# Kernel optimization log

Measured on AMD Instinct MI355X. Metric: run time of the kernel, lower is better.

The kernel has to match this reference:

```python
import jax, jax.numpy as jnp
import numpy as np

N_NODES = 100000
N_EDGES = 1600000
D = 128
NEG_SLOPE = 0.2


def setup_inputs() -> dict:
    key = jax.random.key(0)
    k1, k2, k3, k4, k5, k6 = jax.random.split(key, 6)
    x = jax.random.normal(k1, (N_NODES, D), dtype=jnp.float32)
    src = jax.random.randint(k2, (N_EDGES,), 0, N_NODES)
    dst = jax.random.randint(k3, (N_EDGES,), 0, N_NODES)
    # torch.nn.Linear default init: U(-1/sqrt(fan_in), 1/sqrt(fan_in))
    W = jax.random.uniform(k4, (D, D), dtype=jnp.float32, minval=-1.0, maxval=1.0) / np.sqrt(D)
    a_left = jax.random.uniform(k5, (1, D), dtype=jnp.float32, minval=-1.0, maxval=1.0) / np.sqrt(D)
    a_right = jax.random.uniform(k6, (1, D), dtype=jnp.float32, minval=-1.0, maxval=1.0) / np.sqrt(D)
    return {"x": x, "src": src, "dst": dst, "W": W, "a_left": a_left, "a_right": a_right}


def reference(x, src, dst, W, a_left, a_right):
    n = x.shape[0]
    # node-wise projections
    h = x @ W.T                      # [N, D]
    e_l = h @ a_left.T               # [N, 1]
    e_r = h @ a_right.T              # [N, 1]
    # edge attention logits: u_add_v then leaky_relu
    e = e_l[src] + e_r[dst]          # [E, 1]
    e = jnp.where(e >= 0, e, NEG_SLOPE * e)
    # edge softmax over incoming edges of each destination node
    e = e[:, 0]
    m = jax.ops.segment_max(e, dst, num_segments=n)          # [N]
    m = jnp.where(jnp.isfinite(m), m, 0.0)                   # guard empty segments
    ex = jnp.exp(e - m[dst])                                 # [E]
    denom = jax.ops.segment_sum(ex, dst, num_segments=n)     # [N]
    alpha = ex / jnp.maximum(denom[dst], 1e-38)              # [E]
    # weighted aggregation: sum_e h[src] * alpha -> dst
    msg = h[src] * alpha[:, None]                            # [E, D]
    out = jax.ops.segment_sum(msg, dst, num_segments=n)      # [N, D]
    return out
```

## Files before the change

### kernel.cpp

```cpp
#include <hip/hip_runtime.h>
#include <math.h>

#define N_NODES 100000
#define N_EDGES 1600000
#define D 128
#define NEG_SLOPE_F 0.2f
#define BK 32
#define NB3 3125
#define ECAP 1024
#define BEPB 16384
#define NBINB 98

typedef short short8 __attribute__((ext_vector_type(8)));
typedef float f32x4 __attribute__((ext_vector_type(4)));

__device__ __forceinline__ unsigned short f2bf_rtn(float f) {
    unsigned int u = __float_as_uint(f);
    u += 0x7fffu + ((u >> 16) & 1u);
    return (unsigned short)(u >> 16);
}
__device__ __forceinline__ float bf2f(unsigned short h) {
    return __uint_as_float((unsigned)h << 16);
}

__global__ __launch_bounds__(256) void kbin2(const int* __restrict__ src,
                                             const int* __restrict__ dst,
                                             const float* __restrict__ W,
                                             unsigned short* __restrict__ Wh,
                                             unsigned short* __restrict__ Wl,
                                             unsigned* __restrict__ gcount,
                                             unsigned* __restrict__ binned) {
    if (blockIdx.x == NBINB) {
        for (int i = threadIdx.x; i < D * D; i += 256) {
            float v = W[i];
            unsigned short h = f2bf_rtn(v);
            Wh[i] = h;
            Wl[i] = f2bf_rtn(v - bf2f(h));
        }
        return;
    }
    __shared__ unsigned hist[NB3];
    __shared__ unsigned startb[NB3];
    __shared__ unsigned cnt[NB3];
    int tid = threadIdx.x;
    for (int i = tid; i < NB3; i += 256) { hist[i] = 0; cnt[i] = 0; }
    __syncthreads();
    int base = blockIdx.x * BEPB;
    const int4* d4 = (const int4*)dst;
    const int4* s4 = (const int4*)src;
    int i40 = base >> 2;
    for (int it = 0; it < 16; ++it) {
        int i4 = i40 + it * 256 + tid;
        if (i4 * 4 < N_EDGES) {
            int4 v = d4[i4];
            atomicAdd(&hist[v.x >> 5], 1u);
            atomicAdd(&hist[v.y >> 5], 1u);
            atomicAdd(&hist[v.z >> 5], 1u);
            atomicAdd(&hist[v.w >> 5], 1u);
        }
    }
    __syncthreads();
    for (int b = tid; b < NB3; b += 256) {
        unsigned c = hist[b];
        startb[b] = c ? atomicAdd(&gcount[b], c) : 0u;
    }
    __syncthreads();
    for (int it = 0; it < 16; ++it) {
        int i4 = i40 + it * 256 + tid;
        if (i4 * 4 < N_EDGES) {
            int4 dv = d4[i4];
            int4 sv = s4[i4];
#define PUT(dd, ss)                                                          \
            {                                                                \
                int b = (dd) >> 5;                                           \
                unsigned r = startb[b] + atomicAdd(&cnt[b], 1u);             \
                if (r < ECAP)                                                \
                    binned[(size_t)b * ECAP + r] =                           \
                        ((unsigned)((dd) & 31) << 17) | (unsigned)(ss);      \
            }
            PUT(dv.x, sv.x) PUT(dv.y, sv.y) PUT(dv.z, sv.z) PUT(dv.w, sv.w)
#undef PUT
        }
    }
}

__global__ __launch_bounds__(256) void gemm_mfma2(
        const float* __restrict__ x, const unsigned short* __restrict__ Wh,
        const unsigned short* __restrict__ Wl,
        const float* __restrict__ a_l, const float* __restrict__ a_r,
        unsigned short* __restrict__ hb, float* __restrict__ e_l,
        float* __restrict__ e_r, int n) {
    __shared__ alignas(16) unsigned short Xh[64][136];
    __shared__ alignas(16) unsigned short Bh[64][136];
    __shared__ alignas(16) unsigned short Bl[64][136];
    int tid = threadIdx.x, lane = tid & 63, wid = tid >> 6;
    int p = lane & 15, g = lane >> 4;
    int row0 = blockIdx.x * 64;

    const float4* X4 = (const float4*)x;
    for (int q = 0; q < 8; ++q) {
        int idx = q * 256 + tid;
        int r = idx >> 5, c4 = idx & 31;
        int gr = row0 + r;
        float4 v = (gr < n) ? X4[(size_t)gr * 32 + c4] : make_float4(0.f, 0.f, 0.f, 0.f);
        ushort4 hh;
        hh.x = f2bf_rtn(v.x);
        hh.y = f2bf_rtn(v.y);
        hh.z = f2bf_rtn(v.z);
        hh.w = f2bf_rtn(v.w);
        *(ushort4*)&Xh[r][c4 * 4] = hh;
    }

    f32x4 acc[2][4];
#pragma unroll
    for (int hf = 0; hf < 2; ++hf)
#pragma unroll
        for (int ct = 0; ct < 4; ++ct) acc[hf][ct] = (f32x4)(0.f);

    const uint4* Wh4 = (const uint4*)Wh;
    const uint4* Wl4 = (const uint4*)Wl;
    int arow = wid * 16 + p;

#pragma unroll
    for (int hf = 0; hf < 2; ++hf) {
        __syncthreads();
        for (int q = 0; q < 4; ++q) {
            int idx = q * 256 + tid;
            int r = idx >> 4, c8 = idx & 15;
            *(uint4*)&Bh[r][c8 * 8] = Wh4[((size_t)(hf * 64 + r)) * 16 + c8];
            *(uint4*)&Bl[r][c8 * 8] = Wl4[((size_t)(hf * 64 + r)) * 16 + c8];
        }
        __syncthreads();

#pragma unroll
        for (int kc = 0; kc < 4; ++kc) {
            int cb = kc * 32 + g * 8;
            short8 ah = *(const short8*)&Xh[arow][cb];
#pragma unroll
            for (int ct = 0; ct < 4; ++ct) {
                short8 bh = *(const short8*)&Bh[ct * 16 + p][cb];
                short8 bl = *(const short8*)&Bl[ct * 16 + p][cb];
                acc[hf][ct] = __builtin_amdgcn_mfma_f32_16x16x32_bf16(ah, bh, acc[hf][ct], 0, 0, 0);
                acc[hf][ct] = __builtin_amdgcn_mfma_f32_16x16x32_bf16(ah, bl, acc[hf][ct], 0, 0, 0);
            }
        }
    }

    float al8[2][4], ar8[2][4];
#pragma unroll
    for (int hf = 0; hf < 2; ++hf)
#pragma unroll
        for (int ct = 0; ct < 4; ++ct) {
            al8[hf][ct] = a_l[hf * 64 + ct * 16 + p];
            ar8[hf][ct] = a_r[hf * 64 + ct * 16 + p];
        }
#pragma unroll
    for (int i = 0; i < 4; ++i) {
        int gr = row0 + wid * 16 + g * 4 + i;
        bool ok = gr < n;
        float pl = 0.f, pr = 0.f;
        if (ok) {
#pragma unroll
            for (int hf = 0; hf < 2; ++hf)
#pragma unroll
                for (int ct = 0; ct < 4; ++ct) {
                    float v = acc[hf][ct][i];
                    hb[(size_t)gr * 128 + hf * 64 + ct * 16 + p] = f2bf_rtn(v);
                    pl += v * al8[hf][ct];
                    pr += v * ar8[hf][ct];
                }
        }
#pragma unroll
        for (int o = 8; o; o >>= 1) {
            pl += __shfl_xor(pl, o);
            pr += __shfl_xor(pr, o);
        }
        if (ok && p == 0) { e_l[gr] = pl; e_r[gr] = pr; }
    }
}

__global__ __launch_bounds__(256) void bucket_fused(
        const unsigned short* __restrict__ hb, const float* __restrict__ e_l,
        const float* __restrict__ e_r, const unsigned* __restrict__ gcount,
        const unsigned* __restrict__ binned, float* __restrict__ out) {
    __shared__ unsigned es[ECAP];
    __shared__ float    ee[ECAP];
    __shared__ unsigned short sidx[ECAP];
    __shared__ unsigned cntl[BK];
    __shared__ unsigned startl[BK];
    __shared__ unsigned curl[BK];
    __shared__ float    erl[BK];
    __shared__ int   lds_s[4][64];
    __shared__ float lds_e[4][64];

    int tid = threadIdx.x, lane = tid & 63, w = tid >> 6;
    int g = lane >> 4, p = lane & 15;
    int b = blockIdx.x, d0 = b * BK;
    size_t rs = (size_t)b * ECAP;
    int cnt = min((int)gcount[b], ECAP);

    if (tid < BK) {
        int d = d0 + tid;
        erl[tid] = (d < N_NODES) ? e_r[d] : 0.f;
        cntl[tid] = 0u;
    }
    __syncthreads();

#define ACC8(hv, xe)                                                        \
    acc[0] += xe * __uint_as_float(hv.x << 16);                             \
    acc[1] += xe * __uint_as_float(hv.x & 0xffff0000u);                     \
    acc[2] += xe * __uint_as_float(hv.y << 16);                             \
    acc[3] += xe * __uint_as_float(hv.y & 0xffff0000u);                     \
    acc[4] += xe * __uint_as_float(hv.z << 16);                             \
    acc[5] += xe * __uint_as_float(hv.z & 0xffff0000u);                     \
    acc[6] += xe * __uint_as_float(hv.w << 16);                             \
    acc[7] += xe * __uint_as_float(hv.w & 0xffff0000u);

    for (int i = tid; i < cnt; i += 256) {
        unsigned v = binned[rs + i];
        unsigned ld = v >> 17;
        float e = e_l[v & 0x1ffffu] + erl[ld];
        e = (e >= 0.f) ? e : NEG_SLOPE_F * e;
        es[i] = v;
        ee[i] = __expf(e);
        atomicAdd(&cntl[ld], 1u);
    }
    __syncthreads();
    if (tid < BK) {
        unsigned c = cntl[tid];
        unsigned inc = c;
#pragma unroll
        for (int o = 1; o < BK; o <<= 1) {
            unsigned nv = __shfl_up(inc, o);
            if (lane >= o) inc += nv;
        }
        startl[tid] = inc - c;
        curl[tid] = inc - c;
    }
    __syncthreads();
    for (int i = tid; i < cnt; i += 256) {
        unsigned ld = es[i] >> 17;
        unsigned pos = atomicAdd(&curl[ld], 1u);
        sidx[pos] = (unsigned short)i;
    }
    __syncthreads();
    for (int k = 0; k < BK / 4; ++k) {
        int ld = (k << 2) | w;
        int start = (int)startl[ld];
        int deg = (int)cntl[ld];

        float denom = 0.f;
        float acc[8];
#pragma unroll
        for (int q = 0; q < 8; ++q) acc[q] = 0.f;
        for (int b2 = 0; b2 < deg; b2 += 64) {
            int kk = b2 + lane;
            bool valid = kk < deg;
            int i = valid ? sidx[start + kk] : 0;
            float ex = valid ? ee[i] : 0.f;
            denom += ex;
            lds_s[w][lane] = valid ? (int)(es[i] & 0x1ffffu) : 0;
            lds_e[w][lane] = ex;
            asm volatile("s_waitcnt lgkmcnt(0)" ::: "memory");
            int c2 = min(64, deg - b2);
            int nst = (c2 + 3) >> 2;
            int u = 0;
            for (; u + 4 <= nst; u += 4) {
                int j0 = u * 4 + g;
                int s0 = lds_s[w][j0];       float x0 = lds_e[w][j0];
                int s1 = lds_s[w][j0 + 4];   float x1 = lds_e[w][j0 + 4];
                int s2 = lds_s[w][j0 + 8];   float x2 = lds_e[w][j0 + 8];
                int s3 = lds_s[w][j0 + 12];  float x3 = lds_e[w][j0 + 12];
                uint4 h0 = *(const uint4*)&hb[(size_t)s0 * 128 + p * 8];
                uint4 h1 = *(const uint4*)&hb[(size_t)s1 * 128 + p * 8];
                uint4 h2 = *(const uint4*)&hb[(size_t)s2 * 128 + p * 8];
                uint4 h3 = *(const uint4*)&hb[(size_t)s3 * 128 + p * 8];
                ACC8(h0, x0) ACC8(h1, x1) ACC8(h2, x2) ACC8(h3, x3)
            }
            for (; u < nst; ++u) {
                int j = u * 4 + g;
                int sj = lds_s[w][j];
                float xj = lds_e[w][j];
                uint4 hv = *(const uint4*)&hb[(size_t)sj * 128 + p * 8];
                ACC8(hv, xj)
            }
        }
#pragma unroll
        for (int q = 0; q < 8; ++q) {
            acc[q] += __shfl_xor(acc[q], 16);
            acc[q] += __shfl_xor(acc[q], 32);
        }
#pragma unroll
        for (int o = 32; o; o >>= 1) denom += __shfl_xor(denom, o);
        float inv = 1.f / fmaxf(denom, 1e-38f);
        int d = d0 + ld;
        if (g == 0 && d < N_NODES) {
            f32x4 o0 = {acc[0] * inv, acc[1] * inv, acc[2] * inv, acc[3] * inv};
            f32x4 o1 = {acc[4] * inv, acc[5] * inv, acc[6] * inv, acc[7] * inv};
            __builtin_nontemporal_store(o0, (f32x4*)&out[(size_t)d * 128 + p * 8]);
            __builtin_nontemporal_store(o1, (f32x4*)&out[(size_t)d * 128 + p * 8 + 4]);
        }
    }
#undef ACC8
}

extern "C" void kernel_launch(void* const* d_in, const int* in_sizes, int n_in,
                              void* d_out, int out_size, void* d_ws, size_t ws_size,
                              hipStream_t stream) {
    const float* x   = (const float*)d_in[0];
    const int*   src = (const int*)d_in[1];
    const int*   dst = (const int*)d_in[2];
    const float* W   = (const float*)d_in[3];
    const float* a_l = (const float*)d_in[4];
    const float* a_r = (const float*)d_in[5];
    float* out = (float*)d_out;

    char* ws = (char*)d_ws;
    unsigned short* hb = (unsigned short*)ws; ws += (size_t)N_NODES * D * 2;
    float*    e_l    = (float*)ws;    ws += (size_t)N_NODES * 4;
    float*    e_r    = (float*)ws;    ws += (size_t)N_NODES * 4;
    unsigned short* Wh = (unsigned short*)ws; ws += (size_t)D * D * 2;
    unsigned short* Wl = (unsigned short*)ws; ws += (size_t)D * D * 2;
    unsigned* gcount = (unsigned*)ws; ws += (size_t)NB3 * 4;
    unsigned* binned = (unsigned*)ws; ws += (size_t)NB3 * ECAP * 4;

    hipMemsetAsync(gcount, 0, (size_t)NB3 * 4, stream);

    kbin2<<<NBINB + 1, 256, 0, stream>>>(src, dst, W, Wh, Wl, gcount, binned);
    gemm_mfma2<<<(N_NODES + 63) / 64, 256, 0, stream>>>(x, Wh, Wl, a_l, a_r, hb, e_l, e_r, N_NODES);
    bucket_fused<<<NB3, 256, 0, stream>>>(hb, e_l, e_r, gcount, binned, out);
}
```

Baseline: 137.6 us.

## Fuse edge binning and projection GEMM into one launch with in-block W split

Merges the edge-binning kernel and the MFMA projection GEMM into a single launch, where the first blocks do binning and the rest do GEMM tiles, using shared dynamic LDS. Each GEMM block now converts W from fp32 into bf16 hi/lo parts itself instead of reading a precomputed split, which removes the dependency that forced separate launches. This removes one kernel launch and boundary and lets binning overlap with the GEMM, at the cost of redundant W conversion in every GEMM block and a larger LDS footprint that may limit occupancy.

```diff
diff --git a/kernel.cpp b/kernel.cpp
--- a/kernel.cpp
+++ b/kernel.cpp
@@ -10,6 +10,8 @@
 #define ECAP 1024
 #define BEPB 16384
 #define NBINB 98
+#define NGEMM 1563
+#define DYN_LDS 52224
 
 typedef short short8 __attribute__((ext_vector_type(8)));
 typedef float f32x4 __attribute__((ext_vector_type(4)));
@@ -23,79 +25,69 @@
     return __uint_as_float((unsigned)h << 16);
 }
 
-__global__ __launch_bounds__(256) void kbin2(const int* __restrict__ src,
-                                             const int* __restrict__ dst,
-                                             const float* __restrict__ W,
-                                             unsigned short* __restrict__ Wh,
-                                             unsigned short* __restrict__ Wl,
-                                             unsigned* __restrict__ gcount,
-                                             unsigned* __restrict__ binned) {
-    if (blockIdx.x == NBINB) {
-        for (int i = threadIdx.x; i < D * D; i += 256) {
-            float v = W[i];
-            unsigned short h = f2bf_rtn(v);
-            Wh[i] = h;
-            Wl[i] = f2bf_rtn(v - bf2f(h));
+__global__ __launch_bounds__(256) void fused_prep(
+        const int* __restrict__ src, const int* __restrict__ dst,
+        const float* __restrict__ x, const float* __restrict__ W,
+        const float* __restrict__ a_l, const float* __restrict__ a_r,
+        unsigned* __restrict__ gcount, unsigned* __restrict__ binned,
+        unsigned short* __restrict__ hb, float* __restrict__ e_l,
+        float* __restrict__ e_r) {
+    extern __shared__ __align__(16) char smem[];
+    int tid = threadIdx.x;
+
+    if (blockIdx.x < NBINB) {
+        unsigned* hist   = (unsigned*)smem;
+        unsigned* startb = hist + NB3;
+        unsigned* cnt    = startb + NB3;
+        for (int i = tid; i < NB3; i += 256) { hist[i] = 0; cnt[i] = 0; }
+        __syncthreads();
+        int base = blockIdx.x * BEPB;
+        const int4* d4 = (const int4*)dst;
+        const int4* s4 = (const int4*)src;
+        int i40 = base >> 2;
+        for (int it = 0; it < 16; ++it) {
+            int i4 = i40 + it * 256 + tid;
+            if (i4 * 4 < N_EDGES) {
+                int4 v = d4[i4];
+                atomicAdd(&hist[v.x >> 5], 1u);
+                atomicAdd(&hist[v.y >> 5], 1u);
+                atomicAdd(&hist[v.z >> 5], 1u);
+                atomicAdd(&hist[v.w >> 5], 1u);
+            }
+        }
+        __syncthreads();
+        for (int b = tid; b < NB3; b += 256) {
+            unsigned c = hist[b];
+            startb[b] = c ? atomicAdd(&gcount[b], c) : 0u;
+        }
+        __syncthreads();
+        for (int it = 0; it < 16; ++it) {
+            int i4 = i40 + it * 256 + tid;
+            if (i4 * 4 < N_EDGES) {
+                int4 dv = d4[i4];
+                int4 sv = s4[i4];
+#define PUT(dd, ss)                                                          \
+                {                                                            \
+                    int b = (dd) >> 5;                                       \
+                    unsigned r = startb[b] + atomicAdd(&cnt[b], 1u);         \
+                    if (r < ECAP)                                            \
+                        binned[(size_t)b * ECAP + r] =                       \
+                            ((unsigned)((dd) & 31) << 17) | (unsigned)(ss);  \
+                }
+                PUT(dv.x, sv.x) PUT(dv.y, sv.y) PUT(dv.z, sv.z) PUT(dv.w, sv.w)
+#undef PUT
+            }
         }
         return;
     }
-    __shared__ unsigned hist[NB3];
-    __shared__ unsigned startb[NB3];
-    __shared__ unsigned cnt[NB3];
-    int tid = threadIdx.x;
-    for (int i = tid; i < NB3; i += 256) { hist[i] = 0; cnt[i] = 0; }
-    __syncthreads();
-    int base = blockIdx.x * BEPB;
-    const int4* d4 = (const int4*)dst;
-    const int4* s4 = (const int4*)src;
-    int i40 = base >> 2;
-    for (int it = 0; it < 16; ++it) {
-        int i4 = i40 + it * 256 + tid;
-        if (i4 * 4 < N_EDGES) {
-            int4 v = d4[i4];
-            atomicAdd(&hist[v.x >> 5], 1u);
-            atomicAdd(&hist[v.y >> 5], 1u);
-            atomicAdd(&hist[v.z >> 5], 1u);
-            atomicAdd(&hist[v.w >> 5], 1u);
-        }
-    }
-    __syncthreads();
-    for (int b = tid; b < NB3; b += 256) {
-        unsigned c = hist[b];
-        startb[b] = c ? atomicAdd(&gcount[b], c) : 0u;
-    }
-    __syncthreads();
-    for (int it = 0; it < 16; ++it) {
-        int i4 = i40 + it * 256 + tid;
-        if (i4 * 4 < N_EDGES) {
-            int4 dv = d4[i4];
-            int4 sv = s4[i4];
-#define PUT(dd, ss)                                                          \
-            {                                                                \
-                int b = (dd) >> 5;                                           \
-                unsigned r = startb[b] + atomicAdd(&cnt[b], 1u);             \
-                if (r < ECAP)                                                \
-                    binned[(size_t)b * ECAP + r] =                           \
-                        ((unsigned)((dd) & 31) << 17) | (unsigned)(ss);      \
-            }
-            PUT(dv.x, sv.x) PUT(dv.y, sv.y) PUT(dv.z, sv.z) PUT(dv.w, sv.w)
-#undef PUT
-        }
-    }
-}
-
-__global__ __launch_bounds__(256) void gemm_mfma2(
-        const float* __restrict__ x, const unsigned short* __restrict__ Wh,
-        const unsigned short* __restrict__ Wl,
-        const float* __restrict__ a_l, const float* __restrict__ a_r,
-        unsigned short* __restrict__ hb, float* __restrict__ e_l,
-        float* __restrict__ e_r, int n) {
-    __shared__ alignas(16) unsigned short Xh[64][136];
-    __shared__ alignas(16) unsigned short Bh[64][136];
-    __shared__ alignas(16) unsigned short Bl[64][136];
-    int tid = threadIdx.x, lane = tid & 63, wid = tid >> 6;
+
+    unsigned short (*Xh)[136] = (unsigned short(*)[136])smem;
+    unsigned short (*Bh)[136] = (unsigned short(*)[136])(smem + 17408);
+    unsigned short (*Bl)[136] = (unsigned short(*)[136])(smem + 34816);
+    int lane = tid & 63, wid = tid >> 6;
     int p = lane & 15, g = lane >> 4;
-    int row0 = blockIdx.x * 64;
+    int row0 = (blockIdx.x - NBINB) * 64;
+    int n = N_NODES;
 
     const float4* X4 = (const float4*)x;
     for (int q = 0; q < 8; ++q) {
@@ -117,18 +109,23 @@
 #pragma unroll
         for (int ct = 0; ct < 4; ++ct) acc[hf][ct] = (f32x4)(0.f);
 
-    const uint4* Wh4 = (const uint4*)Wh;
-    const uint4* Wl4 = (const uint4*)Wl;
+    const float4* W4 = (const float4*)W;
     int arow = wid * 16 + p;
 
 #pragma unroll
     for (int hf = 0; hf < 2; ++hf) {
         __syncthreads();
-        for (int q = 0; q < 4; ++q) {
+        for (int q = 0; q < 8; ++q) {
             int idx = q * 256 + tid;
-            int r = idx >> 4, c8 = idx & 15;
-            *(uint4*)&Bh[r][c8 * 8] = Wh4[((size_t)(hf * 64 + r)) * 16 + c8];
-            *(uint4*)&Bl[r][c8 * 8] = Wl4[((size_t)(hf * 64 + r)) * 16 + c8];
+            int r = idx >> 5, c4 = idx & 31;
+            float4 v = W4[((size_t)(hf * 64 + r)) * 32 + c4];
+            ushort4 hh, ll;
+            hh.x = f2bf_rtn(v.x); ll.x = f2bf_rtn(v.x - bf2f(hh.x));
+            hh.y = f2bf_rtn(v.y); ll.y = f2bf_rtn(v.y - bf2f(hh.y));
+            hh.z = f2bf_rtn(v.z); ll.z = f2bf_rtn(v.z - bf2f(hh.z));
+            hh.w = f2bf_rtn(v.w); ll.w = f2bf_rtn(v.w - bf2f(hh.w));
+            *(ushort4*)&Bh[r][c4 * 4] = hh;
+            *(ushort4*)&Bl[r][c4 * 4] = ll;
         }
         __syncthreads();
 
@@ -319,14 +316,12 @@
     unsigned short* hb = (unsigned short*)ws; ws += (size_t)N_NODES * D * 2;
     float*    e_l    = (float*)ws;    ws += (size_t)N_NODES * 4;
     float*    e_r    = (float*)ws;    ws += (size_t)N_NODES * 4;
-    unsigned short* Wh = (unsigned short*)ws; ws += (size_t)D * D * 2;
-    unsigned short* Wl = (unsigned short*)ws; ws += (size_t)D * D * 2;
     unsigned* gcount = (unsigned*)ws; ws += (size_t)NB3 * 4;
     unsigned* binned = (unsigned*)ws; ws += (size_t)NB3 * ECAP * 4;
 
     hipMemsetAsync(gcount, 0, (size_t)NB3 * 4, stream);
 
-    kbin2<<<NBINB + 1, 256, 0, stream>>>(src, dst, W, Wh, Wl, gcount, binned);
-    gemm_mfma2<<<(N_NODES + 63) / 64, 256, 0, stream>>>(x, Wh, Wl, a_l, a_r, hb, e_l, e_r, N_NODES);
+    fused_prep<<<NBINB + NGEMM, 256, DYN_LDS, stream>>>(
+        src, dst, x, W, a_l, a_r, gcount, binned, hb, e_l, e_r);
     bucket_fused<<<NB3, 256, 0, stream>>>(hb, e_l, e_r, gcount, binned, out);
 }
```

After: 117.2 us. -14.8%, faster.
